# Kernel tuning notes

Measured on AMD Instinct MI355X. Metric: run time of the kernel, lower is better.

The kernel has to match this reference:

```python
import jax, jax.numpy as jnp
import numpy as np

N = 16384   # number of samples (sample_idx.shape[0])
H = 512     # hidden_size
D = 128     # input_size
K = 40      # number of observation times
E = 4096    # events per observation time (event_pt blocks made uniform)
DT = 0.05
STEPS_PER_OBS = 2   # obs_times = 2*dt*(1..K) -> exactly 2 Euler steps per obs
EXTRA_STEPS = 10    # prop_to_end Euler steps after last obs (no effect on loss)


def setup_inputs() -> dict:
    key = jax.random.key(0)
    ks = jax.random.split(key, 16)

    X = jax.random.normal(ks[0], (K, E, D), dtype=jnp.float32)
    M = (jax.random.uniform(ks[1], (K, E, D)) < 0.8).astype(jnp.float32)
    # unique sample indices per observation block (torch index-assign assumes
    # no duplicate rows within one event block)
    batch_idx = jax.vmap(lambda k: jax.random.permutation(k, N)[:E])(
        jax.random.split(ks[2], K)).astype(jnp.int32)

    def xavier(k, shape):
        fan_in, fan_out = shape[1], shape[0]
        lim = np.sqrt(6.0 / (fan_in + fan_out))
        return jax.random.uniform(k, shape, jnp.float32, -lim, lim)

    b = lambda n: jnp.full((n,), 0.01, jnp.float32)  # torch bias fill 0.01

    return {
        "X": X, "M": M, "batch_idx": batch_idx,
        # RNNCell params (torch layout: W_ih [H,D], W_hh [H,H])
        "W_ih": xavier(ks[3], (H, D)), "b_ih": b(H),
        "W_hh": xavier(ks[4], (H, H)), "b_hh": b(H),
        # ODEFunc: Linear(H,H) -> tanh -> Linear(H,H)
        "Wo1": xavier(ks[5], (H, H)), "bo1": b(H),
        "Wo2": xavier(ks[6], (H, H)), "bo2": b(H),
        # p_model: Linear(H,H) -> ReLU -> (Dropout p=0, eval) -> Linear(H,D)
        "Wp1": xavier(ks[7], (H, H)), "bp1": b(H),
        "Wp2": xavier(ks[8], (D, H)), "bp2": b(D),
    }


def reference(X, M, batch_idx, W_ih, b_ih, W_hh, b_hh,
              Wo1, bo1, Wo2, bo2, Wp1, bp1, Wp2, bp2):
    def euler(h):
        # h + dt * ODEFunc(h)
        dh = jnp.tanh(h @ Wo1.T + bo1) @ Wo2.T + bo2
        return h + DT * dh

    def p_model(h):
        return jax.nn.relu(h @ Wp1.T + bp1) @ Wp2.T + bp2

    def obs_step(carry, inp):
        h, loss, tot_m = carry
        X_obs, M_obs, i_obs = inp  # [E,D], [E,D], [E]
        # Euler propagation up to this observation time
        for _ in range(STEPS_PER_OBS):
            h = euler(h)
        # MAE loss against prediction p = p_model(h) at observed samples
        p_obs = p_model(h[i_obs])
        loss = loss + jnp.sum(jnp.abs(X_obs - p_obs) * M_obs)
        tot_m = tot_m + jnp.sum(M_obs)
        # RNNCell update (tanh) scattered back into observed rows
        h_new = jnp.tanh(X_obs @ W_ih.T + b_ih + h[i_obs] @ W_hh.T + b_hh)
        h = h.at[i_obs].set(h_new)
        return (h, loss, tot_m), None

    h0 = jnp.zeros((N, H), X.dtype)
    zero = jnp.zeros((), X.dtype)
    (h, loss, tot_m), _ = jax.lax.scan(obs_step, (h0, zero, zero),
                                       (X, M, batch_idx))
    # prop_to_end: extra Euler steps (does not change the returned losses)
    h = jax.lax.fori_loop(0, EXTRA_STEPS, lambda i, hh: euler(hh), h)
    # original returns (loss, loss / total_M_obs); stacked for convenience
    return jnp.stack([loss, loss / tot_m])
```

## Files before the change

kernel.cpp:

```cpp
#include <hip/hip_runtime.h>
#include <hip/hip_bf16.h>
#include <cstddef>
#include <cstdint>

#define NS   16384
#define HS   512
#define DS   128
#define KOBS 40
#define ES   4096
#define DTC  0.05f

typedef __bf16 bf16x8 __attribute__((ext_vector_type(8)));
typedef float  f32x4  __attribute__((ext_vector_type(4)));
typedef __hip_bfloat16 bf16_t;

__device__ __forceinline__ void async16(const void* g, void* l)
{
  __builtin_amdgcn_global_load_lds(
      (const __attribute__((address_space(1))) unsigned int*)g,
      (__attribute__((address_space(3))) unsigned int*)l, 16, 0, 0);
}

__device__ __forceinline__ float fast_tanh(float x)
{
  return 1.f - 2.f / (1.f + __expf(2.f * x));
}

template <int IT, int JT>
__device__ __forceinline__ void mfma_half(
    f32x4 (&acc)[IT][JT], const bf16_t* Ah, const bf16_t* Bh,
    int wr, int wc, int q, int ln)
{
  bf16x8 a[IT], b[JT];
#pragma unroll
  for (int i = 0; i < IT; ++i)
    a[i] = *(const bf16x8*)(Ah + (wr + i * 16 + ln) * 32 + q * 8);
#pragma unroll
  for (int j = 0; j < JT; ++j)
    b[j] = *(const bf16x8*)(Bh + (wc + j * 16 + ln) * 32 + q * 8);
#pragma unroll
  for (int i = 0; i < IT; ++i)
#pragma unroll
    for (int j = 0; j < JT; ++j)
      acc[i][j] = __builtin_amdgcn_mfma_f32_16x16x32_bf16(a[i], b[j], acc[i][j], 0, 0, 0);
}

__device__ __forceinline__ void loop_pre(
    f32x4 (&acc)[4][2],
    const bf16_t* __restrict__ A, const int* __restrict__ idx, int row0,
    const bf16_t* __restrict__ W, int ldw, int col0, int K,
    bf16_t* As, bf16_t* Bs)
{
  const int tid = threadIdx.x, wave = tid >> 6, lane = tid & 63;
  const int q = lane >> 4, ln = lane & 15;
  const int wr = (wave >> 1) * 64, wc = (wave & 1) * 32;
  const int srow = wave * 16 + (lane >> 2);
  const int skc  = (lane & 3) * 8;
  int ar0 = row0 + srow, ar1 = row0 + srow + 64;
  if (idx) { ar0 = idx[ar0]; ar1 = idx[ar1]; }
  const bf16_t* Ap0 = A + (size_t)ar0 * HS + skc;
  const bf16_t* Ap1 = A + (size_t)ar1 * HS + skc;
  const int brow = tid >> 2;
  const bf16_t* Bp = W + (size_t)(col0 + brow) * ldw + skc;
  const int d0 = srow * 32 + skc, d1 = (srow + 64) * 32 + skc;
  const int db = brow * 32 + skc;

  for (int k0 = 0; k0 < K; k0 += 128) {
    __syncthreads();
#pragma unroll
    for (int s = 0; s < 4; ++s) {
      async16(Ap0 + k0 + s * 32, As + s * 4096 + d0);
      async16(Ap1 + k0 + s * 32, As + s * 4096 + d1);
      async16(Bp  + k0 + s * 32, Bs + s * 2048 + db);
    }
    __syncthreads();
#pragma unroll
    for (int s = 0; s < 4; ++s)
      mfma_half<4, 2>(acc, As + s * 4096, Bs + s * 2048, wr, wc, q, ln);
  }
}

__device__ __forceinline__ void loop_post(
    f32x4 (&acc)[2][1],
    const bf16_t* __restrict__ A, int row0,
    const bf16_t* __restrict__ W, int col0, int K,
    bf16_t* As, bf16_t* Bs)
{
  const int tid = threadIdx.x, wave = tid >> 6, lane = tid & 63;
  const int q = lane >> 4, ln = lane & 15;
  const int wr = (wave >> 1) * 32, wc = (wave & 1) * 16;
  const int srow = tid >> 2;
  const int skc  = (tid & 3) * 8;
  const bf16_t* Ap = A + (size_t)(row0 + srow) * HS + skc;
  const int d = srow * 32 + skc;
  const int brow = (tid & 127) >> 2;
  const bf16_t* Bp = W + (size_t)(col0 + brow) * HS + skc;
  const int dbB = brow * 32 + skc;

  for (int k0 = 0; k0 < K; k0 += 64) {
    __syncthreads();
    async16(Ap + k0,      As + d);
    async16(Ap + k0 + 32, As + 2048 + d);
    if (tid < 128) {
      async16(Bp + k0,      Bs + dbB);
      async16(Bp + k0 + 32, Bs + 1024 + dbB);
    }
    __syncthreads();
    mfma_half<2, 1>(acc, As,        Bs,        wr, wc, q, ln);
    mfma_half<2, 1>(acc, As + 2048, Bs + 1024, wr, wc, q, ln);
  }
}

__device__ __forceinline__ void gemm_k512(
    f32x4 (&acc)[4][4], const char* Tb, const bf16_t* __restrict__ Wf,
    int wc, int q, int ln)
{
  const int abase = ln * 1024;
  const int l3 = ln & 7;
  const bf16_t* Wl = Wf + (q * 512 + wc + ln) * 8;
  bf16x8 wA[4], wB[4];
#pragma unroll
  for (int i = 0; i < 4; ++i) wA[i] = *(const bf16x8*)(Wl + i * 128);
#pragma unroll 1
  for (int ks2 = 0; ks2 < 8; ++ks2) {
    {
      const bf16_t* Wk = Wl + (2 * ks2 + 1) * 16384;
#pragma unroll
      for (int i = 0; i < 4; ++i) wB[i] = *(const bf16x8*)(Wk + i * 128);
    }
    {
      bf16x8 t[4];
      const int coff = (((2 * ks2) * 4 + q) ^ l3) << 4;
#pragma unroll
      for (int jb = 0; jb < 4; ++jb)
        t[jb] = *(const bf16x8*)(Tb + jb * 16384 + abase + coff);
#pragma unroll
      for (int i = 0; i < 4; ++i)
#pragma unroll
        for (int jb = 0; jb < 4; ++jb)
          acc[i][jb] = __builtin_amdgcn_mfma_f32_16x16x32_bf16(wA[i], t[jb], acc[i][jb], 0, 0, 0);
    }
    if (ks2 < 7) {
      const bf16_t* Wk = Wl + (2 * ks2 + 2) * 16384;
#pragma unroll
      for (int i = 0; i < 4; ++i) wA[i] = *(const bf16x8*)(Wk + i * 128);
    }
    {
      bf16x8 t[4];
      const int coff = (((2 * ks2 + 1) * 4 + q) ^ l3) << 4;
#pragma unroll
      for (int jb = 0; jb < 4; ++jb)
        t[jb] = *(const bf16x8*)(Tb + jb * 16384 + abase + coff);
#pragma unroll
      for (int i = 0; i < 4; ++i)
#pragma unroll
        for (int jb = 0; jb < 4; ++jb)
          acc[i][jb] = __builtin_amdgcn_mfma_f32_16x16x32_bf16(wB[i], t[jb], acc[i][jb], 0, 0, 0);
    }
  }
}

__global__ __launch_bounds__(512)
__attribute__((amdgpu_waves_per_eu(2, 2)))
void k_euler2(
    bf16_t* __restrict__ h,
    const bf16_t* __restrict__ Wo1, const float* __restrict__ bo1,
    const bf16_t* __restrict__ Wo2, const float* __restrict__ bo2)
{
  __shared__ __align__(16) char Hs[64 * 1024];
  __shared__ __align__(16) char Ts[64 * 1024];
  const int tid = threadIdx.x;
  const int wave = tid >> 6, lane = tid & 63;
  const int q = lane >> 4, ln = lane & 15;
  const int wc = wave * 64;
  const int r0 = blockIdx.x * 64;

#pragma unroll
  for (int u = 0; u < 8; ++u) {
    const int g = u * 512 + tid;
    const int row = g >> 6, c16 = g & 63;
    *(uint4*)(Hs + row * 1024 + ((c16 ^ (row & 7)) << 4)) =
        *(const uint4*)(h + (size_t)(r0 + row) * HS + c16 * 8);
  }
  __syncthreads();

#pragma unroll 1
  for (int step = 0; step < 2; ++step) {
    {
      f32x4 acc[4][4] = {};
      gemm_k512(acc, Hs, Wo1, wc, q, ln);
#pragma unroll
      for (int i = 0; i < 4; ++i) {
        const int c0 = wc + i * 16 + q * 4;
        const float4 b4 = *(const float4*)(bo1 + c0);
        const int cb = c0 * 2;
#pragma unroll
        for (int jb = 0; jb < 4; ++jb) {
          const int row = jb * 16 + ln;
          __attribute__((aligned(8))) bf16_t pk[4];
          pk[0] = __float2bfloat16(fast_tanh(acc[i][jb][0] + b4.x));
          pk[1] = __float2bfloat16(fast_tanh(acc[i][jb][1] + b4.y));
          pk[2] = __float2bfloat16(fast_tanh(acc[i][jb][2] + b4.z));
          pk[3] = __float2bfloat16(fast_tanh(acc[i][jb][3] + b4.w));
          *(uint2*)(Ts + row * 1024 + (((cb >> 4) ^ (row & 7)) << 4) + (cb & 15)) =
              *(const uint2*)pk;
        }
      }
    }
    __syncthreads();
    {
      f32x4 acc[4][4] = {};
      gemm_k512(acc, Ts, Wo2, wc, q, ln);
#pragma unroll
      for (int i = 0; i < 4; ++i) {
        const int c0 = wc + i * 16 + q * 4;
        const float4 b4 = *(const float4*)(bo2 + c0);
        const int cb = c0 * 2;
#pragma unroll
        for (int jb = 0; jb < 4; ++jb) {
          const int row = jb * 16 + ln;
          char* p = Hs + row * 1024 + (((cb >> 4) ^ (row & 7)) << 4) + (cb & 15);
          uint2 ov = *(const uint2*)p;
          const bf16_t* ob = (const bf16_t*)&ov;
          __attribute__((aligned(8))) bf16_t pk[4];
          pk[0] = __float2bfloat16(__bfloat162float(ob[0]) + DTC * (acc[i][jb][0] + b4.x));
          pk[1] = __float2bfloat16(__bfloat162float(ob[1]) + DTC * (acc[i][jb][1] + b4.y));
          pk[2] = __float2bfloat16(__bfloat162float(ob[2]) + DTC * (acc[i][jb][2] + b4.z));
          pk[3] = __float2bfloat16(__bfloat162float(ob[3]) + DTC * (acc[i][jb][3] + b4.w));
          *(uint2*)p = *(const uint2*)pk;
        }
      }
    }
    __syncthreads();
  }

#pragma unroll
  for (int u = 0; u < 8; ++u) {
    const int g = u * 512 + tid;
    const int row = g >> 6, c16 = g & 63;
    *(uint4*)(h + (size_t)(r0 + row) * HS + c16 * 8) =
        *(const uint4*)(Hs + row * 1024 + ((c16 ^ (row & 7)) << 4));
  }
}

__global__ __launch_bounds__(256) void k_obs_pre(
    const bf16_t* __restrict__ h, const int* __restrict__ idx,
    const bf16_t* __restrict__ Wp1, const float* __restrict__ bp1,
    bf16_t* __restrict__ tmpE,
    const float* __restrict__ Xk,
    const bf16_t* __restrict__ Wih, const float* __restrict__ b_ih,
    const bf16_t* __restrict__ Whh, const float* __restrict__ b_hh,
    bf16_t* __restrict__ hnewE)
{
  __shared__ bf16_t As[128 * 128], Bs[64 * 128];
  f32x4 acc[4][2] = {};
  const int tid = threadIdx.x, wave = tid >> 6, lane = tid & 63;
  const int q = lane >> 4, ln = lane & 15;
  const int wr = (wave >> 1) * 64, wc = (wave & 1) * 32;
  const int row0 = blockIdx.x * 128, col0 = blockIdx.y * 64;

  if (blockIdx.z == 0) {
    loop_pre(acc, h, idx, row0, Wp1, HS, col0, HS, As, Bs);
#pragma unroll
    for (int j = 0; j < 2; ++j) {
      const int c = col0 + wc + j * 16 + ln;
      const float bj = bp1[c];
#pragma unroll
      for (int i = 0; i < 4; ++i)
#pragma unroll
        for (int r = 0; r < 4; ++r) {
          const int rw = row0 + wr + i * 16 + q * 4 + r;
          const float v = acc[i][j][r] + bj;
          tmpE[(size_t)rw * HS + c] = __float2bfloat16(v > 0.f ? v : 0.f);
        }
    }
  } else {
    {
      const int brow = tid >> 2;
      const int skc  = (tid & 3) * 8;
      const bf16_t* Bp = Wih + (size_t)(col0 + brow) * DS + skc;
      const int db = brow * 32 + skc;
      const int xr = tid >> 1, xh = (tid & 1) * 16;
#pragma unroll
      for (int s = 0; s < 4; ++s)
        async16(Bp + s * 32, Bs + s * 2048 + db);
#pragma unroll
      for (int s = 0; s < 4; ++s) {
        const float* src = Xk + (size_t)(row0 + xr) * DS + s * 32 + xh;
        __attribute__((aligned(16))) bf16_t buf[16];
#pragma unroll
        for (int u = 0; u < 16; ++u) buf[u] = __float2bfloat16(src[u]);
        *(uint4*)(As + s * 4096 + xr * 32 + xh)     = *(const uint4*)buf;
        *(uint4*)(As + s * 4096 + xr * 32 + xh + 8) = *(const uint4*)(buf + 8);
      }
      __syncthreads();
#pragma unroll
      for (int s = 0; s < 4; ++s)
        mfma_half<4, 2>(acc, As + s * 4096, Bs + s * 2048, wr, wc, q, ln);
    }
    loop_pre(acc, h, idx, row0, Whh, HS, col0, HS, As, Bs);
#pragma unroll
    for (int j = 0; j < 2; ++j) {
      const int c = col0 + wc + j * 16 + ln;
      const float bj = b_ih[c] + b_hh[c];
#pragma unroll
      for (int i = 0; i < 4; ++i)
#pragma unroll
        for (int r = 0; r < 4; ++r) {
          const int rw = row0 + wr + i * 16 + q * 4 + r;
          hnewE[(size_t)rw * HS + c] = __float2bfloat16(fast_tanh(acc[i][j][r] + bj));
        }
    }
  }
}

__global__ __launch_bounds__(256) void k_obs_post(
    const bf16_t* __restrict__ tmpE, const bf16_t* __restrict__ Wp2,
    const float* __restrict__ bp2, const float* __restrict__ X,
    const float* __restrict__ Mm, float* __restrict__ accum,
    bf16_t* __restrict__ h, const bf16_t* __restrict__ hnewE,
    const int* __restrict__ idx)
{
  const int bid = blockIdx.x;
  if (bid >= 256) {
    const int t  = (bid - 256) * 256 + threadIdx.x;
    const int r  = t >> 6;
    const int c8 = (t & 63) * 8;
    const int gr = idx[r];
    *(uint4*)(h + (size_t)gr * HS + c8) = *(const uint4*)(hnewE + (size_t)r * HS + c8);
    return;
  }
  __shared__ bf16_t As[64 * 64], Bs[32 * 64];
  f32x4 acc[2][1] = {};
  const int wave = threadIdx.x >> 6, lane = threadIdx.x & 63;
  const int q = lane >> 4, ln = lane & 15;
  const int wr = (wave >> 1) * 32, wc = (wave & 1) * 16;
  const int row0 = (bid >> 2) * 64, col0 = (bid & 3) * 32;
  loop_post(acc, tmpE, row0, Wp2, col0, HS, As, Bs);
  float ls = 0.f;
  {
    const int c = col0 + wc + ln;
    const float bj = bp2[c];
#pragma unroll
    for (int i = 0; i < 2; ++i)
#pragma unroll
      for (int r = 0; r < 4; ++r) {
        const int rw = row0 + wr + i * 16 + q * 4 + r;
        const float p = acc[i][0][r] + bj;
        const size_t o = (size_t)rw * DS + c;
        ls += fabsf(X[o] - p) * Mm[o];
      }
  }
#pragma unroll
  for (int off = 32; off > 0; off >>= 1) ls += __shfl_down(ls, off);
  __shared__ float red[4];
  if (lane == 0) red[wave] = ls;
  __syncthreads();
  if (threadIdx.x == 0) atomicAdd(accum, red[0] + red[1] + red[2] + red[3]);
}

__global__ void k_cvt(const float* __restrict__ s, bf16_t* __restrict__ d, int n)
{
  const int i = blockIdx.x * 256 + threadIdx.x;
  if (i * 4 < n) {
    const float4 v = ((const float4*)s)[i];
    d[i * 4 + 0] = __float2bfloat16(v.x);
    d[i * 4 + 1] = __float2bfloat16(v.y);
    d[i * 4 + 2] = __float2bfloat16(v.z);
    d[i * 4 + 3] = __float2bfloat16(v.w);
  }
}

__global__ void k_cvt_frag(const float* __restrict__ s, bf16_t* __restrict__ d)
{
  const int t = blockIdx.x * 256 + threadIdx.x;
  const int r = t & 511, c = t >> 9;
  const float4 v0 = *(const float4*)(s + (size_t)r * HS + c * 8);
  const float4 v1 = *(const float4*)(s + (size_t)r * HS + c * 8 + 4);
  __attribute__((aligned(16))) bf16_t buf[8];
  buf[0] = __float2bfloat16(v0.x); buf[1] = __float2bfloat16(v0.y);
  buf[2] = __float2bfloat16(v0.z); buf[3] = __float2bfloat16(v0.w);
  buf[4] = __float2bfloat16(v1.x); buf[5] = __float2bfloat16(v1.y);
  buf[6] = __float2bfloat16(v1.z); buf[7] = __float2bfloat16(v1.w);
  *(uint4*)(d + (size_t)t * 8) = *(const uint4*)buf;
}

__global__ void k_zero(float* __restrict__ p, size_t n4)
{
  size_t i = (size_t)blockIdx.x * blockDim.x + threadIdx.x;
  const size_t st = (size_t)gridDim.x * blockDim.x;
  const float4 z = {0.f, 0.f, 0.f, 0.f};
  for (; i < n4; i += st) ((float4*)p)[i] = z;
}

__global__ void k_zero_accum(float* accum)
{
  if (threadIdx.x < 2) accum[threadIdx.x] = 0.f;
}

__global__ void k_sum(const float* __restrict__ M, size_t n4, float* __restrict__ accum)
{
  __shared__ float red[256];
  float s = 0.f;
  for (size_t i = (size_t)blockIdx.x * blockDim.x + threadIdx.x; i < n4;
       i += (size_t)gridDim.x * blockDim.x) {
    const float4 v = ((const float4*)M)[i];
    s += v.x + v.y + v.z + v.w;
  }
  red[threadIdx.x] = s;
  __syncthreads();
  for (int st = 128; st > 0; st >>= 1) {
    if (threadIdx.x < st) red[threadIdx.x] += red[threadIdx.x + st];
    __syncthreads();
  }
  if (threadIdx.x == 0) atomicAdd(accum + 1, red[0]);
}

__global__ void k_final(const float* __restrict__ accum, float* __restrict__ out)
{
  out[0] = accum[0];
  out[1] = accum[0] / accum[1];
}

extern "C" void kernel_launch(void* const* d_in, const int* in_sizes, int n_in,
                              void* d_out, int out_size, void* d_ws, size_t ws_size,
                              hipStream_t stream)
{
  const float* X    = (const float*)d_in[0];
  const float* M    = (const float*)d_in[1];
  const int*   bidx = (const int*)d_in[2];
  const float* W_ih = (const float*)d_in[3];
  const float* b_ih = (const float*)d_in[4];
  const float* W_hh = (const float*)d_in[5];
  const float* b_hh = (const float*)d_in[6];
  const float* Wo1  = (const float*)d_in[7];
  const float* bo1  = (const float*)d_in[8];
  const float* Wo2  = (const float*)d_in[9];
  const float* bo2  = (const float*)d_in[10];
  const float* Wp1  = (const float*)d_in[11];
  const float* bp1  = (const float*)d_in[12];
  const float* Wp2  = (const float*)d_in[13];
  const float* bp2  = (const float*)d_in[14];
  float* out = (float*)d_out;

  char* w = (char*)d_ws;
  bf16_t* h     = (bf16_t*)w;                         w += (size_t)NS * HS * 2;
  bf16_t* tmpE  = (bf16_t*)w;                         w += (size_t)ES * HS * 2;
  bf16_t* hnewE = (bf16_t*)w;                         w += (size_t)ES * HS * 2;
  bf16_t* wWo1  = (bf16_t*)w;                         w += (size_t)HS * HS * 2;
  bf16_t* wWo2  = (bf16_t*)w;                         w += (size_t)HS * HS * 2;
  bf16_t* wWp1  = (bf16_t*)w;                         w += (size_t)HS * HS * 2;
  bf16_t* wWp2  = (bf16_t*)w;                         w += (size_t)DS * HS * 2;
  bf16_t* wWih  = (bf16_t*)w;                         w += (size_t)HS * DS * 2;
  bf16_t* wWhh  = (bf16_t*)w;                         w += (size_t)HS * HS * 2;
  float*  accum = (float*)w;

  k_zero<<<2048, 256, 0, stream>>>((float*)h, (size_t)NS * HS * 2 / 16);
  k_zero_accum<<<1, 64, 0, stream>>>(accum);
  k_sum<<<2048, 256, 0, stream>>>(M, (size_t)KOBS * ES * DS / 4, accum);
  k_cvt_frag<<<128, 256, 0, stream>>>(Wo1, wWo1);
  k_cvt_frag<<<128, 256, 0, stream>>>(Wo2, wWo2);
  k_cvt<<<256, 256, 0, stream>>>(Wp1, wWp1, HS * HS);
  k_cvt<<<64, 256, 0, stream>>>(Wp2, wWp2, DS * HS);
  k_cvt<<<64, 256, 0, stream>>>(W_ih, wWih, HS * DS);
  k_cvt<<<256, 256, 0, stream>>>(W_hh, wWhh, HS * HS);

  const dim3 gPre(ES / 128, HS / 64, 2);
  const int  gPost = 256 + ES * HS / 8 / 256;

  for (int k = 0; k < KOBS; ++k) {
    const int*   idx = bidx + (size_t)k * ES;
    const float* Xk  = X + (size_t)k * ES * DS;
    const float* Mk  = M + (size_t)k * ES * DS;

    k_euler2<<<NS / 64, 512, 0, stream>>>(h, wWo1, bo1, wWo2, bo2);
    k_obs_pre <<<gPre, 256, 0, stream>>>(h, idx, wWp1, bp1, tmpE,
                                         Xk, wWih, b_ih, wWhh, b_hh, hnewE);
    k_obs_post<<<gPost, 256, 0, stream>>>(tmpE, wWp2, bp2, Xk, Mk, accum,
                                          h, hnewE, idx);
  }

  k_final<<<1, 1, 0, stream>>>(accum, out);
}
```

Measured before the change: 2.841 ms.

## Fold scatter into next Euler load and overlap loss GEMM with next obs

Drops the separate post kernel. The scatter of new hidden rows is replaced by an inverse-index table, built once, that k_euler2 uses to read either hnewE or h while loading its tile. The Wp2 loss GEMM for observation k-1 runs as an extra z-slice of the fused obs kernel for observation k, with tmp double-buffered, and a trailing k_loss handles the last observation. This removes one launch and the scatter pass per observation. It costs an extra inverse table of (K+1)*N ints, an indirect load in the Euler kernel, and the requirement that indices within each block are unique.

```diff
diff --git a/kernel.cpp b/kernel.cpp
--- a/kernel.cpp
+++ b/kernel.cpp
@@ -111,6 +111,37 @@
   }
 }
 
+__device__ __forceinline__ void loss_tile(
+    int t, const bf16_t* __restrict__ tmpP,
+    const bf16_t* __restrict__ Wp2, const float* __restrict__ bp2,
+    const float* __restrict__ X, const float* __restrict__ Mm,
+    float* __restrict__ accum, bf16_t* As, bf16_t* Bs, float* red)
+{
+  f32x4 acc[2][1] = {};
+  const int wave = threadIdx.x >> 6, lane = threadIdx.x & 63;
+  const int q = lane >> 4, ln = lane & 15;
+  const int wr = (wave >> 1) * 32, wc = (wave & 1) * 16;
+  const int row0 = (t >> 2) * 64, col0 = (t & 3) * 32;
+  loop_post(acc, tmpP, row0, Wp2, col0, HS, As, Bs);
+  float ls = 0.f;
+  const int c = col0 + wc + ln;
+  const float bj = bp2[c];
+#pragma unroll
+  for (int i = 0; i < 2; ++i)
+#pragma unroll
+    for (int r = 0; r < 4; ++r) {
+      const int rw = row0 + wr + i * 16 + q * 4 + r;
+      const float p = acc[i][0][r] + bj;
+      const size_t o = (size_t)rw * DS + c;
+      ls += fabsf(X[o] - p) * Mm[o];
+    }
+#pragma unroll
+  for (int off = 32; off > 0; off >>= 1) ls += __shfl_down(ls, off);
+  if (lane == 0) red[wave] = ls;
+  __syncthreads();
+  if (threadIdx.x == 0) atomicAdd(accum, red[0] + red[1] + red[2] + red[3]);
+}
+
 __device__ __forceinline__ void gemm_k512(
     f32x4 (&acc)[4][4], const char* Tb, const bf16_t* __restrict__ Wf,
     int wc, int q, int ln)
@@ -165,7 +196,8 @@
 void k_euler2(
     bf16_t* __restrict__ h,
     const bf16_t* __restrict__ Wo1, const float* __restrict__ bo1,
-    const bf16_t* __restrict__ Wo2, const float* __restrict__ bo2)
+    const bf16_t* __restrict__ Wo2, const float* __restrict__ bo2,
+    const int* __restrict__ invk, const bf16_t* __restrict__ hnewE)
 {
   __shared__ __align__(16) char Hs[64 * 1024];
   __shared__ __align__(16) char Ts[64 * 1024];
@@ -179,8 +211,12 @@
   for (int u = 0; u < 8; ++u) {
     const int g = u * 512 + tid;
     const int row = g >> 6, c16 = g & 63;
+    const int gr = r0 + row;
+    const int iv = invk[gr];
+    const bf16_t* srcp = (iv >= 0) ? (hnewE + (size_t)iv * HS)
+                                   : (h + (size_t)gr * HS);
     *(uint4*)(Hs + row * 1024 + ((c16 ^ (row & 7)) << 4)) =
-        *(const uint4*)(h + (size_t)(r0 + row) * HS + c16 * 8);
+        *(const uint4*)(srcp + c16 * 8);
   }
   __syncthreads();
 
@@ -243,19 +279,32 @@
   }
 }
 
-__global__ __launch_bounds__(256) void k_obs_pre(
+__global__ __launch_bounds__(256) void k_obs_fused(
     const bf16_t* __restrict__ h, const int* __restrict__ idx,
     const bf16_t* __restrict__ Wp1, const float* __restrict__ bp1,
     bf16_t* __restrict__ tmpE,
     const float* __restrict__ Xk,
     const bf16_t* __restrict__ Wih, const float* __restrict__ b_ih,
     const bf16_t* __restrict__ Whh, const float* __restrict__ b_hh,
-    bf16_t* __restrict__ hnewE)
+    bf16_t* __restrict__ hnewE,
+    const bf16_t* __restrict__ tmpPrev,
+    const bf16_t* __restrict__ Wp2, const float* __restrict__ bp2,
+    const float* __restrict__ Xp, const float* __restrict__ Mp,
+    float* __restrict__ accum)
 {
   __shared__ bf16_t As[128 * 128], Bs[64 * 128];
-  f32x4 acc[4][2] = {};
+  __shared__ float red[4];
   const int tid = threadIdx.x, wave = tid >> 6, lane = tid & 63;
   const int q = lane >> 4, ln = lane & 15;
+
+  if (blockIdx.z == 2) {
+    if (Xp == nullptr) return;
+    loss_tile(blockIdx.x * 8 + blockIdx.y, tmpPrev, Wp2, bp2, Xp, Mp,
+              accum, As, Bs, red);
+    return;
+  }
+
+  f32x4 acc[4][2] = {};
   const int wr = (wave >> 1) * 64, wc = (wave & 1) * 32;
   const int row0 = blockIdx.x * 128, col0 = blockIdx.y * 64;
 
@@ -314,49 +363,14 @@
   }
 }
 
-__global__ __launch_bounds__(256) void k_obs_post(
-    const bf16_t* __restrict__ tmpE, const bf16_t* __restrict__ Wp2,
+__global__ __launch_bounds__(256) void k_loss(
+    const bf16_t* __restrict__ tmpP, const bf16_t* __restrict__ Wp2,
     const float* __restrict__ bp2, const float* __restrict__ X,
-    const float* __restrict__ Mm, float* __restrict__ accum,
-    bf16_t* __restrict__ h, const bf16_t* __restrict__ hnewE,
-    const int* __restrict__ idx)
-{
-  const int bid = blockIdx.x;
-  if (bid >= 256) {
-    const int t  = (bid - 256) * 256 + threadIdx.x;
-    const int r  = t >> 6;
-    const int c8 = (t & 63) * 8;
-    const int gr = idx[r];
-    *(uint4*)(h + (size_t)gr * HS + c8) = *(const uint4*)(hnewE + (size_t)r * HS + c8);
-    return;
-  }
+    const float* __restrict__ Mm, float* __restrict__ accum)
+{
   __shared__ bf16_t As[64 * 64], Bs[32 * 64];
-  f32x4 acc[2][1] = {};
-  const int wave = threadIdx.x >> 6, lane = threadIdx.x & 63;
-  const int q = lane >> 4, ln = lane & 15;
-  const int wr = (wave >> 1) * 32, wc = (wave & 1) * 16;
-  const int row0 = (bid >> 2) * 64, col0 = (bid & 3) * 32;
-  loop_post(acc, tmpE, row0, Wp2, col0, HS, As, Bs);
-  float ls = 0.f;
-  {
-    const int c = col0 + wc + ln;
-    const float bj = bp2[c];
-#pragma unroll
-    for (int i = 0; i < 2; ++i)
-#pragma unroll
-      for (int r = 0; r < 4; ++r) {
-        const int rw = row0 + wr + i * 16 + q * 4 + r;
-        const float p = acc[i][0][r] + bj;
-        const size_t o = (size_t)rw * DS + c;
-        ls += fabsf(X[o] - p) * Mm[o];
-      }
-  }
-#pragma unroll
-  for (int off = 32; off > 0; off >>= 1) ls += __shfl_down(ls, off);
   __shared__ float red[4];
-  if (lane == 0) red[wave] = ls;
-  __syncthreads();
-  if (threadIdx.x == 0) atomicAdd(accum, red[0] + red[1] + red[2] + red[3]);
+  loss_tile(blockIdx.x, tmpP, Wp2, bp2, X, Mm, accum, As, Bs, red);
 }
 
 __global__ void k_cvt(const float* __restrict__ s, bf16_t* __restrict__ d, int n)
@@ -396,6 +410,19 @@
 __global__ void k_zero_accum(float* accum)
 {
   if (threadIdx.x < 2) accum[threadIdx.x] = 0.f;
+}
+
+__global__ void k_inv_clear(int* __restrict__ inv, int n)
+{
+  const int i = blockIdx.x * 256 + threadIdx.x;
+  if (i < n) inv[i] = -1;
+}
+
+__global__ void k_inv_build(const int* __restrict__ bidx, int* __restrict__ inv)
+{
+  const int i = blockIdx.x * 256 + threadIdx.x;
+  const int k = i >> 12, e = i & 4095;
+  inv[(size_t)(k + 1) * NS + bidx[i]] = e;
 }
 
 __global__ void k_sum(const float* __restrict__ M, size_t n4, float* __restrict__ accum)
@@ -445,7 +472,8 @@
 
   char* w = (char*)d_ws;
   bf16_t* h     = (bf16_t*)w;                         w += (size_t)NS * HS * 2;
-  bf16_t* tmpE  = (bf16_t*)w;                         w += (size_t)ES * HS * 2;
+  bf16_t* tmpA  = (bf16_t*)w;                         w += (size_t)ES * HS * 2;
+  bf16_t* tmpB  = (bf16_t*)w;                         w += (size_t)ES * HS * 2;
   bf16_t* hnewE = (bf16_t*)w;                         w += (size_t)ES * HS * 2;
   bf16_t* wWo1  = (bf16_t*)w;                         w += (size_t)HS * HS * 2;
   bf16_t* wWo2  = (bf16_t*)w;                         w += (size_t)HS * HS * 2;
@@ -453,10 +481,13 @@
   bf16_t* wWp2  = (bf16_t*)w;                         w += (size_t)DS * HS * 2;
   bf16_t* wWih  = (bf16_t*)w;                         w += (size_t)HS * DS * 2;
   bf16_t* wWhh  = (bf16_t*)w;                         w += (size_t)HS * HS * 2;
+  int*    inv   = (int*)w;                            w += (size_t)(KOBS + 1) * NS * 4;
   float*  accum = (float*)w;
 
   k_zero<<<2048, 256, 0, stream>>>((float*)h, (size_t)NS * HS * 2 / 16);
   k_zero_accum<<<1, 64, 0, stream>>>(accum);
+  k_inv_clear<<<(KOBS + 1) * NS / 256, 256, 0, stream>>>(inv, (KOBS + 1) * NS);
+  k_inv_build<<<KOBS * ES / 256, 256, 0, stream>>>(bidx, inv);
   k_sum<<<2048, 256, 0, stream>>>(M, (size_t)KOBS * ES * DS / 4, accum);
   k_cvt_frag<<<128, 256, 0, stream>>>(Wo1, wWo1);
   k_cvt_frag<<<128, 256, 0, stream>>>(Wo2, wWo2);
@@ -465,20 +496,25 @@
   k_cvt<<<64, 256, 0, stream>>>(W_ih, wWih, HS * DS);
   k_cvt<<<256, 256, 0, stream>>>(W_hh, wWhh, HS * HS);
 
-  const dim3 gPre(ES / 128, HS / 64, 2);
-  const int  gPost = 256 + ES * HS / 8 / 256;
+  const dim3 gObs(ES / 128, HS / 64, 3);
 
   for (int k = 0; k < KOBS; ++k) {
     const int*   idx = bidx + (size_t)k * ES;
     const float* Xk  = X + (size_t)k * ES * DS;
-    const float* Mk  = M + (size_t)k * ES * DS;
-
-    k_euler2<<<NS / 64, 512, 0, stream>>>(h, wWo1, bo1, wWo2, bo2);
-    k_obs_pre <<<gPre, 256, 0, stream>>>(h, idx, wWp1, bp1, tmpE,
-                                         Xk, wWih, b_ih, wWhh, b_hh, hnewE);
-    k_obs_post<<<gPost, 256, 0, stream>>>(tmpE, wWp2, bp2, Xk, Mk, accum,
-                                          h, hnewE, idx);
-  }
+    bf16_t* tcur = (k & 1) ? tmpB : tmpA;
+    const bf16_t* tprev = (k & 1) ? tmpA : tmpB;
+    const float* Xp = k ? X + (size_t)(k - 1) * ES * DS : nullptr;
+    const float* Mp = k ? M + (size_t)(k - 1) * ES * DS : nullptr;
+
+    k_euler2<<<NS / 64, 512, 0, stream>>>(h, wWo1, bo1, wWo2, bo2,
+                                          inv + (size_t)k * NS, hnewE);
+    k_obs_fused<<<gObs, 256, 0, stream>>>(h, idx, wWp1, bp1, tcur,
+                                          Xk, wWih, b_ih, wWhh, b_hh, hnewE,
+                                          tprev, wWp2, bp2, Xp, Mp, accum);
+  }
+  k_loss<<<256, 256, 0, stream>>>(tmpB, wWp2, bp2,
+                                  X + (size_t)(KOBS - 1) * ES * DS,
+                                  M + (size_t)(KOBS - 1) * ES * DS, accum);
 
   k_final<<<1, 1, 0, stream>>>(accum, out);
 }
```

Result: faster. 2.504 ms (-11.9%).
